# Kernel optimization log

Measured on AMD Instinct MI355X. Metric: run time of the kernel, lower is better.

The kernel has to match this reference:

```python
import jax, jax.numpy as jnp
import numpy as np

HEADS = 8
DIM_HEAD = 64
INNER = HEADS * DIM_HEAD  # 512
EPS = 1e-6


def layer_norm(x, gamma, beta):
    mu = jnp.mean(x, axis=-1, keepdims=True)
    var = jnp.var(x, axis=-1, keepdims=True)
    return (x - mu) * jax.lax.rsqrt(var + EPS) * gamma + beta


def setup_inputs() -> dict:
    key = jax.random.key(0)
    ks = jax.random.split(key, 8)
    b, n = 2, 2048
    s = lambda d: 1.0 / np.sqrt(d)
    return {
        "x": jax.random.normal(ks[0], (b, n, INNER), dtype=jnp.float32),
        # weights stored input-major: y = x @ W
        "w_qkv": jax.random.normal(ks[1], (INNER, 3 * INNER), dtype=jnp.float32) * s(INNER),
        "w_out": jax.random.normal(ks[2], (INNER, INNER), dtype=jnp.float32) * s(INNER),
        "b_out": jax.random.normal(ks[3], (INNER,), dtype=jnp.float32) * 0.01,
        "w_ff1": jax.random.normal(ks[4], (INNER, 4 * INNER), dtype=jnp.float32) * s(INNER),
        "w_ff2": jax.random.normal(ks[5], (4 * INNER, INNER), dtype=jnp.float32) * s(4 * INNER),
        "g1": jnp.ones((INNER,), dtype=jnp.float32),
        "be1": jnp.zeros((INNER,), dtype=jnp.float32),
        "g2": jnp.ones((INNER,), dtype=jnp.float32),
        "be2": jnp.zeros((INNER,), dtype=jnp.float32),
    }


def reference(x, w_qkv, w_out, b_out, w_ff1, w_ff2, g1, be1, g2, be2):
    b, n, _ = x.shape
    scale = DIM_HEAD ** (-0.5)
    qkv = x @ w_qkv  # [b, n, 3*inner]
    qkv = qkv.reshape(b, n, 3, HEADS, DIM_HEAD)
    q = qkv[:, :, 0].transpose(0, 2, 1, 3)  # [b, h, n, d]
    k = qkv[:, :, 1].transpose(0, 2, 1, 3)
    v = qkv[:, :, 2].transpose(0, 2, 1, 3)
    dots = jnp.einsum('bhqd,bhkd->bhqk', q, k) * scale
    attn = jax.nn.softmax(dots, axis=-1)
    out = jnp.einsum('bhqk,bhkd->bhqd', attn, v)
    out = out.transpose(0, 2, 1, 3).reshape(b, n, INNER)
    out = out @ w_out + b_out
    attn_res = layer_norm(x + out, g1, be1)
    # NOTE: no activation between the two FFN linears (faithful to source)
    ff = (attn_res @ w_ff1) @ w_ff2
    return layer_norm(attn_res + ff, g2, be2)
```

## Files before the change

### kernel.cpp

```cpp
#include <hip/hip_runtime.h>
#include <hip/hip_bf16.h>
#include <cstdint>
#include <cstddef>
#include <math.h>

#define HEADS 8
#define DHEAD 64
#define INNER 512
#define BATCH 2
#define SEQ   2048
#define MROWS (BATCH*SEQ)
#define LN_EPS 1e-6f
#define KSPLIT 4
#define KCHUNK (SEQ/KSPLIT)
#define QSCALE 0.18033688011110918f

typedef unsigned short u16;
typedef __attribute__((ext_vector_type(8))) short short8;
typedef __attribute__((ext_vector_type(4))) short short4v;
typedef __attribute__((ext_vector_type(4))) float f32x4;

#define MFMA16(a,b,c) __builtin_amdgcn_mfma_f32_16x16x32_bf16((a),(b),(c),0,0,0)
#if __has_builtin(__builtin_amdgcn_mfma_f32_16x16x16bf16_1k)
#define HAVE_MFMA16K16 1
#define MFMA16K16(a,b,c) __builtin_amdgcn_mfma_f32_16x16x16bf16_1k((a),(b),(c),0,0,0)
#endif

__device__ __forceinline__ float bf2f(u16 u) {
    union { float f; uint32_t i; } x; x.i = ((uint32_t)u) << 16; return x.f;
}
__device__ __forceinline__ u16 f2bf(float f) {
    __hip_bfloat16 h = __float2bfloat16(f);
    return *reinterpret_cast<u16*>(&h);
}
__device__ __forceinline__ void gl_lds16(const void* g, void* l) {
    __builtin_amdgcn_global_load_lds(
        (const __attribute__((address_space(1))) void*)g,
        (__attribute__((address_space(3))) void*)l, 16, 0, 0);
}

__global__ void prep_kernel(const float* __restrict__ x, u16* __restrict__ x_b,
                            const float* __restrict__ w_qkv, u16* __restrict__ w_qkvT,
                            const float* __restrict__ w_out, u16* __restrict__ w_outT,
                            const float* __restrict__ w_ff1, u16* __restrict__ w_ff1T,
                            const float* __restrict__ w_ff2, u16* __restrict__ w_ff2T) {
    __shared__ float T[32][33];
    const int blk = blockIdx.x, tid = threadIdx.x;
    if (blk < 2048) {
        int i = blk * 256 + tid;
        float4 v = reinterpret_cast<const float4*>(x)[i];
        ushort4 o;
        o.x = f2bf(v.x); o.y = f2bf(v.y); o.z = f2bf(v.z); o.w = f2bf(v.w);
        reinterpret_cast<ushort4*>(x_b)[i] = o;
        return;
    }
    const float* B; u16* Bt; int K, N, t;
    if (blk < 2816)      { B = w_qkv; Bt = w_qkvT; K = 512;  N = 1536; t = blk - 2048; }
    else if (blk < 3072) { B = w_out; Bt = w_outT; K = 512;  N = 512;  t = blk - 2816; }
    else if (blk < 4096) { B = w_ff1; Bt = w_ff1T; K = 512;  N = 2048; t = blk - 3072; }
    else                 { B = w_ff2; Bt = w_ff2T; K = 2048; N = 512;  t = blk - 4096; }
    const int nb = N / 32;
    const int n0 = (t % nb) * 32, k0 = (t / nb) * 32;
    const int r = tid >> 3, c = (tid & 7) * 4;
    float4 v = *reinterpret_cast<const float4*>(&B[(size_t)(k0 + r) * N + n0 + c]);
    T[c + 0][r] = v.x; T[c + 1][r] = v.y; T[c + 2][r] = v.z; T[c + 3][r] = v.w;
    __syncthreads();
    ushort4 o;
    o.x = f2bf(T[r][c + 0]); o.y = f2bf(T[r][c + 1]);
    o.z = f2bf(T[r][c + 2]); o.w = f2bf(T[r][c + 3]);
    *reinterpret_cast<ushort4*>(&Bt[(size_t)(n0 + r) * K + k0 + c]) = o;
}

template<int BN, int BK, int EPI>
__global__ __launch_bounds__(256) void gemm_bt(const u16* __restrict__ A,
                                               const u16* __restrict__ Bt,
                                               const float* __restrict__ bias,
                                               float* __restrict__ C,
                                               u16* __restrict__ Cb,
                                               u16* __restrict__ Vt,
                                               int M, int N, int K) {
    constexpr int WN = BN / 2;
    constexpr int NT = WN / 16;
    constexpr int ACH = 128 * BK / 8;
    constexpr int BCH = BN * BK / 8;
    constexpr int CW = BK / 8;
    __shared__ u16 As[128 * BK];
    __shared__ u16 Bs[BN * BK];
    const int tid = threadIdx.x;
    const int wave = tid >> 6, lane = tid & 63;
    const int l15 = lane & 15, quad = lane >> 4;
    const int wm = (wave >> 1) * 64, wn = (wave & 1) * WN;
    const int row0 = blockIdx.y * 128, col0 = blockIdx.x * BN;

    int kbase = 0, kend = K;
    if (EPI == 3) {
        int chunk = K / gridDim.z;
        kbase = blockIdx.z * chunk; kend = kbase + chunk;
    }

    f32x4 acc[4][NT];
    #pragma unroll
    for (int mi = 0; mi < 4; ++mi)
        #pragma unroll
        for (int ni = 0; ni < NT; ++ni)
            #pragma unroll
            for (int e = 0; e < 4; ++e) acc[mi][ni][e] = 0.f;

    for (int k0 = kbase; k0 < kend; k0 += BK) {
        #pragma unroll
        for (int idx0 = 0; idx0 < ACH + BCH; idx0 += 256) {
            int idx = idx0 + tid;
            if (idx < ACH) {
                int r = idx / CW, ic = (idx % CW) * 8;
                gl_lds16(A + (size_t)(row0 + r) * K + k0 + ic, &As[idx * 8]);
            } else {
                int ib = idx - ACH;
                int r = ib / CW, ic = (ib % CW) * 8;
                gl_lds16(Bt + (size_t)(col0 + r) * K + k0 + ic, &Bs[ib * 8]);
            }
        }
        __syncthreads();

        #pragma unroll
        for (int ks2 = 0; ks2 < BK / 32; ++ks2) {
            short8 af[4], bfr[NT];
            #pragma unroll
            for (int mi = 0; mi < 4; ++mi)
                af[mi] = *reinterpret_cast<const short8*>(
                    &As[(wm + mi * 16 + l15) * BK + ks2 * 32 + quad * 8]);
            #pragma unroll
            for (int ni = 0; ni < NT; ++ni)
                bfr[ni] = *reinterpret_cast<const short8*>(
                    &Bs[(wn + ni * 16 + l15) * BK + ks2 * 32 + quad * 8]);
            #pragma unroll
            for (int mi = 0; mi < 4; ++mi)
                #pragma unroll
                for (int ni = 0; ni < NT; ++ni)
                    acc[mi][ni] = MFMA16(af[mi], bfr[ni], acc[mi][ni]);
        }
        __syncthreads();
    }

    #pragma unroll
    for (int mi = 0; mi < 4; ++mi)
        #pragma unroll
        for (int ni = 0; ni < NT; ++ni) {
            const int cc = col0 + wn + ni * 16 + l15;
            const int rr0 = row0 + wm + mi * 16 + quad * 4;
            if (EPI == 0) {
                #pragma unroll
                for (int r = 0; r < 4; ++r)
                    Cb[(size_t)(rr0 + r) * N + cc] = f2bf(acc[mi][ni][r]);
            } else if (EPI == 1) {
                #pragma unroll
                for (int r = 0; r < 4; ++r)
                    C[(size_t)(rr0 + r) * N + cc] = acc[mi][ni][r] + bias[cc];
            } else if (EPI == 3) {
                u16* Cz = Cb + (size_t)blockIdx.z * M * N;
                #pragma unroll
                for (int r = 0; r < 4; ++r)
                    Cz[(size_t)(rr0 + r) * N + cc] = f2bf(acc[mi][ni][r]);
            } else {
                if (cc < 1024) {
                    const bool isq = (cc < 512);
                    size_t base = isq ? (size_t)cc
                                      : ((size_t)MROWS * 512 + cc - 512);
                    const float sc = isq ? QSCALE : 1.f;
                    #pragma unroll
                    for (int r = 0; r < 4; ++r)
                        Cb[base + (size_t)(rr0 + r) * 512] = f2bf(acc[mi][ni][r] * sc);
                } else {
                    int hh = (cc - 1024) >> 6, dd = (cc - 1024) & 63;
                    int bb = rr0 >> 11, srow = rr0 & 2047;
                    ushort4 o;
                    o.x = f2bf(acc[mi][ni][0]); o.y = f2bf(acc[mi][ni][1]);
                    o.z = f2bf(acc[mi][ni][2]); o.w = f2bf(acc[mi][ni][3]);
                    *reinterpret_cast<ushort4*>(
                        &Vt[(((size_t)(bb * 8 + hh) * 64 + dd) << 11) + srow]) = o;
                }
            }
        }
}

__global__ __launch_bounds__(256) void attn_kernel(const u16* __restrict__ qk_b,
                                                   const u16* __restrict__ vT_b,
                                                   u16* __restrict__ OpartB,
                                                   float* __restrict__ lpart) {
    __shared__ u16 SM[2 * 64 * 64 + 2 * 64 * 72];
    u16 (*Qs)[64] = (u16(*)[64])SM;
    u16 (*Ks)[72] = (u16(*)[72])(SM + 2 * 64 * 64);
    u16 (*VT)[72] = (u16(*)[72])(SM + 2 * 64 * 64 + 64 * 72);

    const int tid = threadIdx.x;
    const int wave = tid >> 6, lane = tid & 63;
    const int l15 = lane & 15, quad = lane >> 4;
    const int qt = blockIdx.x, bh = blockIdx.y, ks = blockIdx.z;
    const int b = bh >> 3, h = bh & 7;
    const int w16 = wave * 16;
    const int r0 = tid >> 3, r1 = r0 + 32;
    const int ch = (tid & 7) * 8;

    {
        const u16* qb = qk_b + (size_t)(b * SEQ + qt * 128) * 512 + h * 64;
        #pragma unroll
        for (int j = 0; j < 4; ++j) {
            int idx = tid + j * 256;
            int r = idx >> 3, c = (idx & 7) * 8;
            *reinterpret_cast<uint4*>(&Qs[r][c]) =
                *reinterpret_cast<const uint4*>(&qb[(size_t)r * 512 + c]);
        }
    }
    __syncthreads();

    short8 qf[2][2];
    #pragma unroll
    for (int t = 0; t < 2; ++t) {
        qf[t][0] = *reinterpret_cast<const short8*>(&Qs[t * 64 + w16 + l15][quad * 8]);
        qf[t][1] = *reinterpret_cast<const short8*>(&Qs[t * 64 + w16 + l15][32 + quad * 8]);
    }

    const u16* kb = qk_b + (size_t)MROWS * 512
                  + (size_t)(b * SEQ + ks * KCHUNK) * 512 + h * 64;
    const u16* vb = vT_b + (size_t)bh * 64 * 2048 + ks * KCHUNK;

    uint4 kr0 = *reinterpret_cast<const uint4*>(&kb[(size_t)r0 * 512 + ch]);
    uint4 kr1 = *reinterpret_cast<const uint4*>(&kb[(size_t)r1 * 512 + ch]);
    uint4 vr0 = *reinterpret_cast<const uint4*>(&vb[(size_t)r0 * 2048 + ch]);
    uint4 vr1 = *reinterpret_cast<const uint4*>(&vb[(size_t)r1 * 2048 + ch]);

#ifdef HAVE_MFMA16K16
    f32x4 oacc[2][4];
    float lsum[2] = {0.f, 0.f};
    #pragma unroll
    for (int t = 0; t < 2; ++t)
        #pragma unroll
        for (int di = 0; di < 4; ++di)
            #pragma unroll
            for (int e = 0; e < 4; ++e) oacc[t][di][e] = 0.f;

    for (int kt = 0; kt < KCHUNK / 64; ++kt) {
        *reinterpret_cast<uint4*>(&Ks[r0][ch]) = kr0;
        *reinterpret_cast<uint4*>(&Ks[r1][ch]) = kr1;
        *reinterpret_cast<uint4*>(&VT[r0][ch]) = vr0;
        *reinterpret_cast<uint4*>(&VT[r1][ch]) = vr1;
        __syncthreads();

        if (kt + 1 < KCHUNK / 64) {
            const u16* kb2 = kb + (size_t)(kt + 1) * 64 * 512;
            const u16* vb2 = vb + (kt + 1) * 64;
            kr0 = *reinterpret_cast<const uint4*>(&kb2[(size_t)r0 * 512 + ch]);
            kr1 = *reinterpret_cast<const uint4*>(&kb2[(size_t)r1 * 512 + ch]);
            vr0 = *reinterpret_cast<const uint4*>(&vb2[(size_t)r0 * 2048 + ch]);
            vr1 = *reinterpret_cast<const uint4*>(&vb2[(size_t)r1 * 2048 + ch]);
        }

        short8 kf[4];
        #pragma unroll
        for (int ni = 0; ni < 4; ++ni)
            kf[ni] = *reinterpret_cast<const short8*>(&Ks[ni * 16 + l15][quad * 8]);
        short8 kf2[4];
        #pragma unroll
        for (int ni = 0; ni < 4; ++ni)
            kf2[ni] = *reinterpret_cast<const short8*>(&Ks[ni * 16 + l15][32 + quad * 8]);

        #pragma unroll
        for (int t = 0; t < 2; ++t) {
            f32x4 sacc[4];
            #pragma unroll
            for (int ni = 0; ni < 4; ++ni)
                #pragma unroll
                for (int e = 0; e < 4; ++e) sacc[ni][e] = 0.f;
            #pragma unroll
            for (int ni = 0; ni < 4; ++ni)
                sacc[ni] = MFMA16(kf[ni], qf[t][0], sacc[ni]);
            #pragma unroll
            for (int ni = 0; ni < 4; ++ni)
                sacc[ni] = MFMA16(kf2[ni], qf[t][1], sacc[ni]);

            #pragma unroll
            for (int ni = 0; ni < 4; ++ni) {
                float p0 = exp2f(sacc[ni][0]);
                float p1 = exp2f(sacc[ni][1]);
                float p2 = exp2f(sacc[ni][2]);
                float p3 = exp2f(sacc[ni][3]);
                lsum[t] += (p0 + p1) + (p2 + p3);
                union { short4v v; uint32_t u[2]; } P;
                P.u[0] = __builtin_amdgcn_perm(__float_as_uint(p1),
                                               __float_as_uint(p0), 0x07060302u);
                P.u[1] = __builtin_amdgcn_perm(__float_as_uint(p3),
                                               __float_as_uint(p2), 0x07060302u);
                #pragma unroll
                for (int di = 0; di < 4; ++di) {
                    short4v vf = *reinterpret_cast<const short4v*>(
                        &VT[di * 16 + l15][ni * 16 + quad * 4]);
                    oacc[t][di] = MFMA16K16(vf, P.v, oacc[t][di]);
                }
            }
        }
        __syncthreads();
    }

    #pragma unroll
    for (int t = 0; t < 2; ++t) {
        lsum[t] += __shfl_xor(lsum[t], 16);
        lsum[t] += __shfl_xor(lsum[t], 32);
    }

    const size_t pbase = ((size_t)(ks * 16 + bh) * SEQ + qt * 128);
    if (lane < 16) {
        lpart[pbase + w16 + lane] = lsum[0];
        lpart[pbase + 64 + w16 + lane] = lsum[1];
    }

    float* OTf = (float*)SM;
    const int ql = tid >> 2, dseg = (tid & 3) * 16;
    #pragma unroll
    for (int t = 0; t < 2; ++t) {
        __syncthreads();
        #pragma unroll
        for (int di = 0; di < 4; ++di)
            #pragma unroll
            for (int r = 0; r < 4; ++r)
                OTf[(di * 16 + quad * 4 + r) * 68 + w16 + l15] = oacc[t][di][r];
        __syncthreads();
        u16 ov[16];
        #pragma unroll
        for (int i = 0; i < 16; ++i) ov[i] = f2bf(OTf[(dseg + i) * 68 + ql]);
        u16* op = &OpartB[(pbase + t * 64 + ql) * 64 + dseg];
        *reinterpret_cast<uint4*>(op)     = *reinterpret_cast<const uint4*>(ov);
        *reinterpret_cast<uint4*>(op + 8) = *reinterpret_cast<const uint4*>(ov + 8);
    }
#else
    f32x4 oacc[2][4];
    float lsum[2][4];
    #pragma unroll
    for (int t = 0; t < 2; ++t)
        #pragma unroll
        for (int di = 0; di < 4; ++di) {
            #pragma unroll
            for (int e = 0; e < 4; ++e) oacc[t][di][e] = 0.f;
            lsum[t][di] = 0.f;
        }

    for (int kt = 0; kt < KCHUNK / 64; ++kt) {
        *reinterpret_cast<uint4*>(&Ks[r0][ch]) = kr0;
        *reinterpret_cast<uint4*>(&Ks[r1][ch]) = kr1;
        *reinterpret_cast<uint4*>(&VT[r0][ch]) = vr0;
        *reinterpret_cast<uint4*>(&VT[r1][ch]) = vr1;
        __syncthreads();

        if (kt + 1 < KCHUNK / 64) {
            const u16* kb2 = kb + (size_t)(kt + 1) * 64 * 512;
            const u16* vb2 = vb + (kt + 1) * 64;
            kr0 = *reinterpret_cast<const uint4*>(&kb2[(size_t)r0 * 512 + ch]);
            kr1 = *reinterpret_cast<const uint4*>(&kb2[(size_t)r1 * 512 + ch]);
            vr0 = *reinterpret_cast<const uint4*>(&vb2[(size_t)r0 * 2048 + ch]);
            vr1 = *reinterpret_cast<const uint4*>(&vb2[(size_t)r1 * 2048 + ch]);
        }

        #pragma unroll
        for (int t = 0; t < 2; ++t) {
            f32x4 sacc[4];
            #pragma unroll
            for (int ni = 0; ni < 4; ++ni)
                #pragma unroll
                for (int e = 0; e < 4; ++e) sacc[ni][e] = 0.f;
            #pragma unroll
            for (int ksk = 0; ksk < 2; ++ksk) {
                short8 kf[4];
                #pragma unroll
                for (int ni = 0; ni < 4; ++ni)
                    kf[ni] = *reinterpret_cast<const short8*>(
                        &Ks[ni * 16 + l15][ksk * 32 + quad * 8]);
                #pragma unroll
                for (int ni = 0; ni < 4; ++ni)
                    sacc[ni] = MFMA16(qf[t][ksk], kf[ni], sacc[ni]);
            }
            #pragma unroll
            for (int ni = 0; ni < 4; ++ni)
                #pragma unroll
                for (int r = 0; r < 4; ++r) {
                    float p = exp2f(sacc[ni][r]);
                    lsum[t][r] += p;
                    Qs[t * 64 + w16 + quad * 4 + r][ni * 16 + l15] = f2bf(p);
                }
            #pragma unroll
            for (int ksk = 0; ksk < 2; ++ksk) {
                short8 pf = *reinterpret_cast<const short8*>(
                    &Qs[t * 64 + w16 + l15][ksk * 32 + quad * 8]);
                #pragma unroll
                for (int di = 0; di < 4; ++di) {
                    short8 vf = *reinterpret_cast<const short8*>(
                        &VT[di * 16 + l15][ksk * 32 + quad * 8]);
                    oacc[t][di] = MFMA16(pf, vf, oacc[t][di]);
                }
            }
        }
        __syncthreads();
    }

    const size_t pbase = ((size_t)(ks * 16 + bh) * SEQ + qt * 128);
    #pragma unroll
    for (int t = 0; t < 2; ++t) {
        #pragma unroll
        for (int r = 0; r < 4; ++r) {
            float v = lsum[t][r];
            v += __shfl_xor(v, 1); v += __shfl_xor(v, 2);
            v += __shfl_xor(v, 4); v += __shfl_xor(v, 8);
            lsum[t][r] = v;
        }
        #pragma unroll
        for (int di = 0; di < 4; ++di)
            #pragma unroll
            for (int r = 0; r < 4; ++r)
                OpartB[(pbase + t * 64 + w16 + quad * 4 + r) * 64 + di * 16 + l15]
                    = f2bf(oacc[t][di][r]);
        if (l15 == 0)
            #pragma unroll
            for (int r = 0; r < 4; ++r)
                lpart[pbase + t * 64 + w16 + quad * 4 + r] = lsum[t][r];
    }
#endif
}

__global__ void attn_combine_kernel(const u16* __restrict__ OpartB,
                                    const float* __restrict__ lpart,
                                    u16* __restrict__ attn_b) {
    int i = blockIdx.x * 256 + threadIdx.x;
    int e = i * 4;
    int row = e >> 9;
    int c = e & 511;
    int h = c >> 6, d = c & 63;
    int b = row >> 11, srow = row & 2047;
    int bh = b * 8 + h;

    float ax = 0.f, ay = 0.f, az = 0.f, aw = 0.f, l = 0.f;
    #pragma unroll
    for (int ks = 0; ks < KSPLIT; ++ks) {
        size_t pk = (size_t)(ks * 16 + bh) * SEQ + srow;
        ushort4 o = *reinterpret_cast<const ushort4*>(&OpartB[pk * 64 + d]);
        ax += bf2f(o.x); ay += bf2f(o.y); az += bf2f(o.z); aw += bf2f(o.w);
        l += lpart[pk];
    }
    float li = 1.f / l;
    ushort4 o;
    o.x = f2bf(ax * li); o.y = f2bf(ay * li);
    o.z = f2bf(az * li); o.w = f2bf(aw * li);
    *reinterpret_cast<ushort4*>(&attn_b[(size_t)row * INNER + c]) = o;
}

template<bool A16, bool S16, bool TWO>
__global__ __launch_bounds__(256) void ln_kernel(const void* __restrict__ a_,
                                                 const void* __restrict__ s0_,
                                                 const void* __restrict__ s1_,
                                                 const float* __restrict__ g,
                                                 const float* __restrict__ be,
                                                 float* __restrict__ out32,
                                                 u16* __restrict__ out16) {
    const int tid = threadIdx.x, wave = tid >> 6, lane = tid & 63;
    const int row = blockIdx.x * 4 + wave;
    const size_t off = (size_t)row * INNER;

    float v[8];
    #pragma unroll
    for (int j = 0; j < 2; ++j) {
        const int c = j * 256 + lane * 4;
        float a0, a1, a2, a3;
        if (A16) {
            ushort4 u = *reinterpret_cast<const ushort4*>((const u16*)a_ + off + c);
            a0 = bf2f(u.x); a1 = bf2f(u.y); a2 = bf2f(u.z); a3 = bf2f(u.w);
        } else {
            float4 u = *reinterpret_cast<const float4*>((const float*)a_ + off + c);
            a0 = u.x; a1 = u.y; a2 = u.z; a3 = u.w;
        }
        float s0, s1, s2, s3;
        if (S16) {
            ushort4 u = *reinterpret_cast<const ushort4*>((const u16*)s0_ + off + c);
            s0 = bf2f(u.x); s1 = bf2f(u.y); s2 = bf2f(u.z); s3 = bf2f(u.w);
        } else {
            float4 u = *reinterpret_cast<const float4*>((const float*)s0_ + off + c);
            s0 = u.x; s1 = u.y; s2 = u.z; s3 = u.w;
        }
        v[j*4+0] = a0 + s0; v[j*4+1] = a1 + s1; v[j*4+2] = a2 + s2; v[j*4+3] = a3 + s3;
        if (TWO) {
            if (S16) {
                ushort4 u = *reinterpret_cast<const ushort4*>((const u16*)s1_ + off + c);
                v[j*4+0] += bf2f(u.x); v[j*4+1] += bf2f(u.y);
                v[j*4+2] += bf2f(u.z); v[j*4+3] += bf2f(u.w);
            } else {
                float4 u = *reinterpret_cast<const float4*>((const float*)s1_ + off + c);
                v[j*4+0] += u.x; v[j*4+1] += u.y; v[j*4+2] += u.z; v[j*4+3] += u.w;
            }
        }
    }

    float s = 0.f;
    #pragma unroll
    for (int i = 0; i < 8; ++i) s += v[i];
    #pragma unroll
    for (int m = 1; m < 64; m <<= 1) s += __shfl_xor(s, m);
    const float mu = s * (1.f / INNER);

    float q = 0.f;
    #pragma unroll
    for (int i = 0; i < 8; ++i) { v[i] -= mu; q += v[i] * v[i]; }
    #pragma unroll
    for (int m = 1; m < 64; m <<= 1) q += __shfl_xor(q, m);
    const float rstd = rsqrtf(q * (1.f / INNER) + LN_EPS);

    #pragma unroll
    for (int j = 0; j < 2; ++j) {
        const int c = j * 256 + lane * 4;
        float4 gv = *reinterpret_cast<const float4*>(g + c);
        float4 bv = *reinterpret_cast<const float4*>(be + c);
        float y0 = v[j*4+0] * rstd * gv.x + bv.x;
        float y1 = v[j*4+1] * rstd * gv.y + bv.y;
        float y2 = v[j*4+2] * rstd * gv.z + bv.z;
        float y3 = v[j*4+3] * rstd * gv.w + bv.w;
        if (out32) {
            float4 o = {y0, y1, y2, y3};
            *reinterpret_cast<float4*>(out32 + off + c) = o;
        }
        if (out16) {
            ushort4 o;
            o.x = f2bf(y0); o.y = f2bf(y1); o.z = f2bf(y2); o.w = f2bf(y3);
            *reinterpret_cast<ushort4*>(out16 + off + c) = o;
        }
    }
}

extern "C" void kernel_launch(void* const* d_in, const int* in_sizes, int n_in,
                              void* d_out, int out_size, void* d_ws, size_t ws_size,
                              hipStream_t stream) {
    const float* x     = (const float*)d_in[0];
    const float* w_qkv = (const float*)d_in[1];
    const float* w_out = (const float*)d_in[2];
    const float* b_out = (const float*)d_in[3];
    const float* w_ff1 = (const float*)d_in[4];
    const float* w_ff2 = (const float*)d_in[5];
    const float* g1    = (const float*)d_in[6];
    const float* be1   = (const float*)d_in[7];
    const float* g2    = (const float*)d_in[8];
    const float* be2   = (const float*)d_in[9];
    float* out = (float*)d_out;

    char* W = (char*)d_ws;
    u16*   w_outT     = (u16*)  (W + 0);
    u16*   w_ff1T     = (u16*)  (W + 524288);
    u16*   w_ff2T     = (u16*)  (W + 2621440);
    u16*   qk_b       = (u16*)  (W + 4718592);
    float* proj       = (float*)(W + 4718592);
    u16*   ff2p       = (u16*)  (W + 4718592);
    u16*   vT_b       = (u16*)  (W + 13107200);
    u16*   attn_res_b = (u16*)  (W + 13107200);
    u16*   x_b        = (u16*)  (W + 17301504);
    u16*   w_qkvT     = (u16*)  (W + 21495808);
    u16*   OpartB     = (u16*)  (W + 17301504);
    u16*   ff1_b      = (u16*)  (W + 17301504);
    float* lpart      = (float*)(W + 34078720);
    u16*   attn_b     = (u16*)  (W + 34603008);

    prep_kernel<<<5120, 256, 0, stream>>>(x, x_b, w_qkv, w_qkvT, w_out, w_outT,
                                          w_ff1, w_ff1T, w_ff2, w_ff2T);

    gemm_bt<64, 64, 2><<<dim3(1536 / 64, MROWS / 128), 256, 0, stream>>>(
        x_b, w_qkvT, nullptr, nullptr, qk_b, vT_b, MROWS, 1536, INNER);

    attn_kernel<<<dim3(SEQ / 128, BATCH * HEADS, KSPLIT), 256, 0, stream>>>(
        qk_b, vT_b, OpartB, lpart);

    attn_combine_kernel<<<(MROWS * INNER / 4) / 256, 256, 0, stream>>>(
        OpartB, lpart, attn_b);

    gemm_bt<64, 64, 1><<<dim3(INNER / 64, MROWS / 128), 256, 0, stream>>>(
        attn_b, w_outT, b_out, proj, nullptr, nullptr, MROWS, INNER, INNER);

    ln_kernel<false, false, false><<<MROWS / 4, 256, 0, stream>>>(
        x, proj, nullptr, g1, be1, nullptr, attn_res_b);

    gemm_bt<128, 64, 0><<<dim3(2048 / 128, MROWS / 128), 256, 0, stream>>>(
        attn_res_b, w_ff1T, nullptr, nullptr, ff1_b, nullptr, MROWS, 2048, INNER);

    gemm_bt<64, 64, 3><<<dim3(INNER / 64, MROWS / 128, 2), 256, 0, stream>>>(
        ff1_b, w_ff2T, nullptr, nullptr, ff2p, nullptr, MROWS, INNER, 2048);

    ln_kernel<true, true, true><<<MROWS / 4, 256, 0, stream>>>(
        attn_res_b, ff2p, ff2p + (size_t)MROWS * INNER, g2, be2, out, nullptr);
}
```

Baseline: 206.8 us.

## Split-K out-proj and FF2 GEMMs, move softmax row sums onto MFMA

The output-projection GEMM now uses split-K with 2 partial bf16 slices and FF2 uses 4 slices instead of 2. The layer-norm kernel sums the slices and adds the bias, which was previously applied in the GEMM epilogue. This raises block count on small-N GEMMs to fill more compute units, at the cost of extra partial-sum traffic and bf16 rounding of the partials. In the attention kernel, per-row exp sums are now computed with an MFMA against a ones vector instead of scalar adds plus shuffles. This takes VALU work off the exp loop but sums bf16-rounded probabilities.

```diff
diff --git a/kernel.cpp b/kernel.cpp
--- a/kernel.cpp
+++ b/kernel.cpp
@@ -74,8 +74,6 @@
 template<int BN, int BK, int EPI>
 __global__ __launch_bounds__(256) void gemm_bt(const u16* __restrict__ A,
                                                const u16* __restrict__ Bt,
-                                               const float* __restrict__ bias,
-                                               float* __restrict__ C,
                                                u16* __restrict__ Cb,
                                                u16* __restrict__ Vt,
                                                int M, int N, int K) {
@@ -151,10 +149,6 @@
                 #pragma unroll
                 for (int r = 0; r < 4; ++r)
                     Cb[(size_t)(rr0 + r) * N + cc] = f2bf(acc[mi][ni][r]);
-            } else if (EPI == 1) {
-                #pragma unroll
-                for (int r = 0; r < 4; ++r)
-                    C[(size_t)(rr0 + r) * N + cc] = acc[mi][ni][r] + bias[cc];
             } else if (EPI == 3) {
                 u16* Cz = Cb + (size_t)blockIdx.z * M * N;
                 #pragma unroll
@@ -229,14 +223,19 @@
     uint4 vr1 = *reinterpret_cast<const uint4*>(&vb[(size_t)r1 * 2048 + ch]);
 
 #ifdef HAVE_MFMA16K16
-    f32x4 oacc[2][4];
-    float lsum[2] = {0.f, 0.f};
-    #pragma unroll
-    for (int t = 0; t < 2; ++t)
+    const short ONEB = (short)0x3F80;
+    const short4v ones = {ONEB, ONEB, ONEB, ONEB};
+
+    f32x4 oacc[2][4], lacc[2];
+    #pragma unroll
+    for (int t = 0; t < 2; ++t) {
         #pragma unroll
         for (int di = 0; di < 4; ++di)
             #pragma unroll
             for (int e = 0; e < 4; ++e) oacc[t][di][e] = 0.f;
+        #pragma unroll
+        for (int e = 0; e < 4; ++e) lacc[t][e] = 0.f;
+    }
 
     for (int kt = 0; kt < KCHUNK / 64; ++kt) {
         *reinterpret_cast<uint4*>(&Ks[r0][ch]) = kr0;
@@ -254,14 +253,12 @@
             vr1 = *reinterpret_cast<const uint4*>(&vb2[(size_t)r1 * 2048 + ch]);
         }
 
-        short8 kf[4];
-        #pragma unroll
-        for (int ni = 0; ni < 4; ++ni)
-            kf[ni] = *reinterpret_cast<const short8*>(&Ks[ni * 16 + l15][quad * 8]);
-        short8 kf2[4];
-        #pragma unroll
-        for (int ni = 0; ni < 4; ++ni)
+        short8 kf[4], kf2[4];
+        #pragma unroll
+        for (int ni = 0; ni < 4; ++ni) {
+            kf[ni]  = *reinterpret_cast<const short8*>(&Ks[ni * 16 + l15][quad * 8]);
             kf2[ni] = *reinterpret_cast<const short8*>(&Ks[ni * 16 + l15][32 + quad * 8]);
+        }
 
         #pragma unroll
         for (int t = 0; t < 2; ++t) {
@@ -283,12 +280,12 @@
                 float p1 = exp2f(sacc[ni][1]);
                 float p2 = exp2f(sacc[ni][2]);
                 float p3 = exp2f(sacc[ni][3]);
-                lsum[t] += (p0 + p1) + (p2 + p3);
                 union { short4v v; uint32_t u[2]; } P;
                 P.u[0] = __builtin_amdgcn_perm(__float_as_uint(p1),
                                                __float_as_uint(p0), 0x07060302u);
                 P.u[1] = __builtin_amdgcn_perm(__float_as_uint(p3),
                                                __float_as_uint(p2), 0x07060302u);
+                lacc[t] = MFMA16K16(ones, P.v, lacc[t]);
                 #pragma unroll
                 for (int di = 0; di < 4; ++di) {
                     short4v vf = *reinterpret_cast<const short4v*>(
@@ -300,16 +297,10 @@
         __syncthreads();
     }
 
-    #pragma unroll
-    for (int t = 0; t < 2; ++t) {
-        lsum[t] += __shfl_xor(lsum[t], 16);
-        lsum[t] += __shfl_xor(lsum[t], 32);
-    }
-
     const size_t pbase = ((size_t)(ks * 16 + bh) * SEQ + qt * 128);
     if (lane < 16) {
-        lpart[pbase + w16 + lane] = lsum[0];
-        lpart[pbase + 64 + w16 + lane] = lsum[1];
+        lpart[pbase + w16 + lane]      = lacc[0][0];
+        lpart[pbase + 64 + w16 + lane] = lacc[1][0];
     }
 
     float* OTf = (float*)SM;
@@ -449,10 +440,11 @@
     *reinterpret_cast<ushort4*>(&attn_b[(size_t)row * INNER + c]) = o;
 }
 
-template<bool A16, bool S16, bool TWO>
+template<bool A16, int NS>
 __global__ __launch_bounds__(256) void ln_kernel(const void* __restrict__ a_,
-                                                 const void* __restrict__ s0_,
-                                                 const void* __restrict__ s1_,
+                                                 const u16* __restrict__ s_,
+                                                 size_t sstride,
+                                                 const float* __restrict__ bias,
                                                  const float* __restrict__ g,
                                                  const float* __restrict__ be,
                                                  float* __restrict__ out32,
@@ -465,32 +457,24 @@
     #pragma unroll
     for (int j = 0; j < 2; ++j) {
         const int c = j * 256 + lane * 4;
-        float a0, a1, a2, a3;
         if (A16) {
             ushort4 u = *reinterpret_cast<const ushort4*>((const u16*)a_ + off + c);
-            a0 = bf2f(u.x); a1 = bf2f(u.y); a2 = bf2f(u.z); a3 = bf2f(u.w);
+            v[j*4+0] = bf2f(u.x); v[j*4+1] = bf2f(u.y);
+            v[j*4+2] = bf2f(u.z); v[j*4+3] = bf2f(u.w);
         } else {
             float4 u = *reinterpret_cast<const float4*>((const float*)a_ + off + c);
-            a0 = u.x; a1 = u.y; a2 = u.z; a3 = u.w;
-        }
-        float s0, s1, s2, s3;
-        if (S16) {
-            ushort4 u = *reinterpret_cast<const ushort4*>((const u16*)s0_ + off + c);
-            s0 = bf2f(u.x); s1 = bf2f(u.y); s2 = bf2f(u.z); s3 = bf2f(u.w);
-        } else {
-            float4 u = *reinterpret_cast<const float4*>((const float*)s0_ + off + c);
-            s0 = u.x; s1 = u.y; s2 = u.z; s3 = u.w;
-        }
-        v[j*4+0] = a0 + s0; v[j*4+1] = a1 + s1; v[j*4+2] = a2 + s2; v[j*4+3] = a3 + s3;
-        if (TWO) {
-            if (S16) {
-                ushort4 u = *reinterpret_cast<const ushort4*>((const u16*)s1_ + off + c);
-                v[j*4+0] += bf2f(u.x); v[j*4+1] += bf2f(u.y);
-                v[j*4+2] += bf2f(u.z); v[j*4+3] += bf2f(u.w);
-            } else {
-                float4 u = *reinterpret_cast<const float4*>((const float*)s1_ + off + c);
-                v[j*4+0] += u.x; v[j*4+1] += u.y; v[j*4+2] += u.z; v[j*4+3] += u.w;
-            }
+            v[j*4+0] = u.x; v[j*4+1] = u.y; v[j*4+2] = u.z; v[j*4+3] = u.w;
+        }
+        #pragma unroll
+        for (int s = 0; s < NS; ++s) {
+            ushort4 u = *reinterpret_cast<const ushort4*>(
+                s_ + (size_t)s * sstride + off + c);
+            v[j*4+0] += bf2f(u.x); v[j*4+1] += bf2f(u.y);
+            v[j*4+2] += bf2f(u.z); v[j*4+3] += bf2f(u.w);
+        }
+        if (bias) {
+            float4 u = *reinterpret_cast<const float4*>(bias + c);
+            v[j*4+0] += u.x; v[j*4+1] += u.y; v[j*4+2] += u.z; v[j*4+3] += u.w;
         }
     }
 
@@ -549,8 +533,7 @@
     u16*   w_ff1T     = (u16*)  (W + 524288);
     u16*   w_ff2T     = (u16*)  (W + 2621440);
     u16*   qk_b       = (u16*)  (W + 4718592);
-    float* proj       = (float*)(W + 4718592);
-    u16*   ff2p       = (u16*)  (W + 4718592);
+    u16*   projp      = (u16*)  (W + 4718592);
     u16*   vT_b       = (u16*)  (W + 13107200);
     u16*   attn_res_b = (u16*)  (W + 13107200);
     u16*   x_b        = (u16*)  (W + 17301504);
@@ -559,12 +542,13 @@
     u16*   ff1_b      = (u16*)  (W + 17301504);
     float* lpart      = (float*)(W + 34078720);
     u16*   attn_b     = (u16*)  (W + 34603008);
+    u16*   ff2p       = (u16*)  (W + 38797312);
 
     prep_kernel<<<5120, 256, 0, stream>>>(x, x_b, w_qkv, w_qkvT, w_out, w_outT,
                                           w_ff1, w_ff1T, w_ff2, w_ff2T);
 
     gemm_bt<64, 64, 2><<<dim3(1536 / 64, MROWS / 128), 256, 0, stream>>>(
-        x_b, w_qkvT, nullptr, nullptr, qk_b, vT_b, MROWS, 1536, INNER);
+        x_b, w_qkvT, qk_b, vT_b, MROWS, 1536, INNER);
 
     attn_kernel<<<dim3(SEQ / 128, BATCH * HEADS, KSPLIT), 256, 0, stream>>>(
         qk_b, vT_b, OpartB, lpart);
@@ -572,18 +556,18 @@
     attn_combine_kernel<<<(MROWS * INNER / 4) / 256, 256, 0, stream>>>(
         OpartB, lpart, attn_b);
 
-    gemm_bt<64, 64, 1><<<dim3(INNER / 64, MROWS / 128), 256, 0, stream>>>(
-        attn_b, w_outT, b_out, proj, nullptr, nullptr, MROWS, INNER, INNER);
-
-    ln_kernel<false, false, false><<<MROWS / 4, 256, 0, stream>>>(
-        x, proj, nullptr, g1, be1, nullptr, attn_res_b);
+    gemm_bt<64, 64, 3><<<dim3(INNER / 64, MROWS / 128, 2), 256, 0, stream>>>(
+        attn_b, w_outT, projp, nullptr, MROWS, INNER, INNER);
+
+    ln_kernel<false, 2><<<MROWS / 4, 256, 0, stream>>>(
+        x, projp, (size_t)MROWS * INNER, b_out, g1, be1, nullptr, attn_res_b);
 
     gemm_bt<128, 64, 0><<<dim3(2048 / 128, MROWS / 128), 256, 0, stream>>>(
-        attn_res_b, w_ff1T, nullptr, nullptr, ff1_b, nullptr, MROWS, 2048, INNER);
-
-    gemm_bt<64, 64, 3><<<dim3(INNER / 64, MROWS / 128, 2), 256, 0, stream>>>(
-        ff1_b, w_ff2T, nullptr, nullptr, ff2p, nullptr, MROWS, INNER, 2048);
-
-    ln_kernel<true, true, true><<<MROWS / 4, 256, 0, stream>>>(
-        attn_res_b, ff2p, ff2p + (size_t)MROWS * INNER, g2, be2, out, nullptr);
-}
+        attn_res_b, w_ff1T, ff1_b, nullptr, MROWS, 2048, INNER);
+
+    gemm_bt<64, 64, 3><<<dim3(INNER / 64, MROWS / 128, 4), 256, 0, stream>>>(
+        ff1_b, w_ff2T, ff2p, nullptr, MROWS, INNER, 2048);
+
+    ln_kernel<true, 4><<<MROWS / 4, 256, 0, stream>>>(
+        attn_res_b, ff2p, (size_t)MROWS * INNER, nullptr, g2, be2, out, nullptr);
+}
```

New measurement: 203.9 us. No clear change (-1.4%).
